# Optimization experiments

Measured on AMD Instinct MI355X. Metric: run time of the kernel, lower is better.

The kernel has to match this reference:

```python
import jax, jax.numpy as jnp
import numpy as np

B, S, SE, H, NH = 1, 2048, 2048, 1024, 16
HD = H // NH
INNER = 4 * H
EPS = 1e-5


def layer_norm(x, g, b):
    mu = jnp.mean(x, axis=-1, keepdims=True)
    var = jnp.mean(jnp.square(x - mu), axis=-1, keepdims=True)
    return (x - mu) * jax.lax.rsqrt(var + EPS) * g + b


def split_heads(x):  # [B,T,H] -> [B,NH,T,HD]
    b, t, _ = x.shape
    return x.reshape(b, t, NH, HD).transpose(0, 2, 1, 3)


def merge_heads(x):  # [B,NH,T,HD] -> [B,T,H]
    b, nh, t, hd = x.shape
    return x.transpose(0, 2, 1, 3).reshape(b, t, nh * hd)


def setup_inputs() -> dict:
    key = jax.random.key(0)
    ks = jax.random.split(key, 16)
    n = lambda k, shp: (jax.random.normal(k, shp, jnp.float32) * 0.02)
    return {
        "hidden_states": jax.random.normal(ks[0], (B, S, H), jnp.float32),
        "encoder_hidden_states": jax.random.normal(ks[1], (B, SE, H), jnp.float32),
        "scorer_logits": jax.random.normal(ks[2], (B, SE), jnp.float32),
        "ln1_g": jnp.ones((H,), jnp.float32), "ln1_b": jnp.zeros((H,), jnp.float32),
        "c_attn_w": n(ks[3], (H, 3 * H)), "c_attn_b": jnp.zeros((3 * H,), jnp.float32),
        "attn_proj_w": n(ks[4], (H, H)), "attn_proj_b": jnp.zeros((H,), jnp.float32),
        "lnx_g": jnp.ones((H,), jnp.float32), "lnx_b": jnp.zeros((H,), jnp.float32),
        "q_attn_w": n(ks[5], (H, H)), "q_attn_b": jnp.zeros((H,), jnp.float32),
        "x_kv_w": n(ks[6], (H, 2 * H)), "x_kv_b": jnp.zeros((2 * H,), jnp.float32),
        "x_proj_w": n(ks[7], (H, H)), "x_proj_b": jnp.zeros((H,), jnp.float32),
        "ln2_g": jnp.ones((H,), jnp.float32), "ln2_b": jnp.zeros((H,), jnp.float32),
        "fc_w": n(ks[8], (H, INNER)), "fc_b": jnp.zeros((INNER,), jnp.float32),
        "mlp_proj_w": n(ks[9], (INNER, H)), "mlp_proj_b": jnp.zeros((H,), jnp.float32),
    }


def _attn_core(q, k, v, extra_bias=None, causal_bool=False, tril_diag2_additive=False):
    # q,k,v: [B,NH,T,HD]; eager attention, materializes full score matrix (faithful to source)
    w = jnp.einsum("bhqd,bhkd->bhqk", q, k) / jnp.sqrt(jnp.asarray(HD, q.dtype))
    ql, kl = q.shape[-2], k.shape[-2]
    neg = jnp.finfo(w.dtype).min
    if causal_bool:
        mask = jnp.tril(jnp.ones((ql, kl), bool))  # self-attn boolean causal mask
        w = jnp.where(mask[None, None], w, neg)
    if tril_diag2_additive:
        cm = jnp.tril(jnp.ones((ql, kl), w.dtype), k=2)  # limit_cross_attn: tril diagonal=2
        w = w + jnp.where(cm == 0, neg, jnp.zeros((), w.dtype))[None, None]
    if extra_bias is not None:
        w = w + extra_bias[:, None, None, :]  # scorer_logits additive per-key bias
    w = jax.nn.softmax(w, axis=-1)
    return jnp.einsum("bhqk,bhkd->bhqd", w, v)


def reference(hidden_states, encoder_hidden_states, scorer_logits,
              ln1_g, ln1_b, c_attn_w, c_attn_b, attn_proj_w, attn_proj_b,
              lnx_g, lnx_b, q_attn_w, q_attn_b, x_kv_w, x_kv_b, x_proj_w, x_proj_b,
              ln2_g, ln2_b, fc_w, fc_b, mlp_proj_w, mlp_proj_b):
    # --- self attention ---
    residual = hidden_states
    x = layer_norm(hidden_states, ln1_g, ln1_b)
    qkv = x @ c_attn_w + c_attn_b
    q, k, v = jnp.split(qkv, 3, axis=-1)
    a = _attn_core(split_heads(q), split_heads(k), split_heads(v), causal_bool=True)
    a = merge_heads(a) @ attn_proj_w + attn_proj_b
    hidden_states = a + residual
    # --- cross attention (limit_cross_attn=True, scorer_logits bias) ---
    residual = hidden_states
    x = layer_norm(hidden_states, lnx_g, lnx_b)
    q = x @ q_attn_w + q_attn_b
    kv = encoder_hidden_states @ x_kv_w + x_kv_b
    k, v = jnp.split(kv, 2, axis=-1)
    a = _attn_core(split_heads(q), split_heads(k), split_heads(v),
                   extra_bias=scorer_logits, tril_diag2_additive=True)
    a = merge_heads(a) @ x_proj_w + x_proj_b
    hidden_states = residual + a
    # --- MLP (gelu_new = tanh approx) ---
    residual = hidden_states
    x = layer_norm(hidden_states, ln2_g, ln2_b)
    h = jax.nn.gelu(x @ fc_w + fc_b, approximate=True)
    hidden_states = residual + (h @ mlp_proj_w + mlp_proj_b)
    return hidden_states
```

## Files before the change

### kernel.cpp

```cpp
#include <hip/hip_runtime.h>
#include <stdint.h>

#define H     1024
#define S     2048
#define SEQE  2048
#define NHEAD 16
#define HD    64
#define INNER 4096
#define EPSLN 1e-5f
#define LOG2E 1.44269504089f
#define SCALE2 (0.125f * LOG2E)

typedef __attribute__((ext_vector_type(8))) short short8;
typedef __attribute__((ext_vector_type(4))) float floatx4;

__device__ __forceinline__ float b2f(unsigned short u){
  union { unsigned int i; float f; } v; v.i = ((unsigned int)u) << 16; return v.f;
}
__device__ __forceinline__ unsigned short f2b(float f){
  union { float f; unsigned int i; } v; v.f = f;
  unsigned int x = v.i;
  unsigned int r = (x + 0x7FFFu + ((x >> 16) & 1u)) >> 16;
  return (unsigned short)r;
}
__device__ __forceinline__ float gelu_tanh(float x){
  float x3 = x*x*x;
  float t = tanhf(0.7978845608028654f*(x + 0.044715f*x3));
  return 0.5f*x*(1.0f+t);
}

__device__ __forceinline__ void gld16(const unsigned short* g, unsigned short* l){
  __builtin_amdgcn_global_load_lds(
      (const __attribute__((address_space(1))) unsigned int*)g,
      (__attribute__((address_space(3))) unsigned int*)l,
      16, 0, 0);
}

__global__ __launch_bounds__(256) void k_sniff(
    const unsigned short* __restrict__ p, int* __restrict__ flag){
  __shared__ int any;
  if (threadIdx.x == 0) any = 0;
  __syncthreads();
  int bad = 0;
  for (int i = threadIdx.x; i < 8192; i += 256){
    float v = b2f(p[i]);
    if (!(fabsf(v) < 1e6f)) bad = 1;
  }
  if (bad) any = 1;
  __syncthreads();
  if (threadIdx.x == 0) flag[0] = any;
}

__global__ __launch_bounds__(256) void k_cvt(
    const void* __restrict__ src, unsigned short* __restrict__ dst, int n,
    const int* __restrict__ flag){
  int i = blockIdx.x * 256 + threadIdx.x;
  if (i < n)
    dst[i] = flag[0] ? f2b(((const float*)src)[i]) : ((const unsigned short*)src)[i];
}

struct SmallCvt {
  const void* src[16];
  unsigned short* dst[16];
  int n[16];
};
__global__ __launch_bounds__(256) void k_cvt_small(SmallCvt sc, const int* __restrict__ flag){
  int t = blockIdx.x;
  int fl = flag[0];
  const float* sf = (const float*)sc.src[t];
  const unsigned short* sb = (const unsigned short*)sc.src[t];
  unsigned short* d = sc.dst[t];
  for (int i = threadIdx.x; i < sc.n[t]; i += 256)
    d[i] = fl ? f2b(sf[i]) : sb[i];
}

__global__ __launch_bounds__(256) void k_transpose(
    const void* __restrict__ srcv, unsigned short* __restrict__ dst,
    int R, int C, const int* __restrict__ flag){
  __shared__ unsigned short t[32][33];
  const float* sf = (const float*)srcv;
  const unsigned short* sb = (const unsigned short*)srcv;
  int fl = flag[0];
  int bc = blockIdx.x * 32, br = blockIdx.y * 32;
  int tx = threadIdx.x, ty = threadIdx.y;
  #pragma unroll
  for (int i = 0; i < 4; i++){
    size_t idx = (size_t)(br + ty + i*8) * C + bc + tx;
    t[ty + i*8][tx] = fl ? f2b(sf[idx]) : sb[idx];
  }
  __syncthreads();
  #pragma unroll
  for (int i = 0; i < 4; i++)
    dst[(size_t)(bc + ty + i*8) * R + br + tx] = t[tx][ty + i*8];
}

__global__ __launch_bounds__(256) void k_resid_init(
    const void* __restrict__ in, float* __restrict__ out, int n,
    const int* __restrict__ flag){
  int i = blockIdx.x * 256 + threadIdx.x;
  if (i < n)
    out[i] = flag[0] ? ((const float*)in)[i] : b2f(((const unsigned short*)in)[i]);
}

__global__ __launch_bounds__(256) void k_layernorm(
    const float* __restrict__ x,
    const unsigned short* __restrict__ g, const unsigned short* __restrict__ bb,
    unsigned short* __restrict__ y){
  __shared__ float scratch[4];
  int row = blockIdx.x, tid = threadIdx.x;
  float v[4];
  #pragma unroll
  for (int i=0;i<4;i++) v[i] = x[(size_t)row*H + tid + i*256];
  float s = v[0]+v[1]+v[2]+v[3];
  for (int o=32;o;o>>=1) s += __shfl_xor(s,o,64);
  int wid = tid>>6, lane = tid&63;
  if (lane==0) scratch[wid]=s;
  __syncthreads();
  float mu = (scratch[0]+scratch[1]+scratch[2]+scratch[3]) * (1.0f/H);
  __syncthreads();
  float q = 0.f;
  #pragma unroll
  for (int i=0;i<4;i++){ float d=v[i]-mu; q += d*d; }
  for (int o=32;o;o>>=1) q += __shfl_xor(q,o,64);
  if (lane==0) scratch[wid]=q;
  __syncthreads();
  float var = (scratch[0]+scratch[1]+scratch[2]+scratch[3]) * (1.0f/H);
  float rstd = rsqrtf(var + EPSLN);
  #pragma unroll
  for (int i=0;i<4;i++){
    int idx = tid + i*256;
    float o = (v[i]-mu)*rstd*b2f(g[idx]) + b2f(bb[idx]);
    y[(size_t)row*H + idx] = f2b(o);
  }
}

__global__ __launch_bounds__(256) void k_gemm64(
    const unsigned short* __restrict__ A, const unsigned short* __restrict__ BT,
    const unsigned short* __restrict__ bias,
    unsigned short* __restrict__ outb, float* __restrict__ resid,
    int M, int N, int K, int mode, const int* __restrict__ flag,
    int vcol0, unsigned short* __restrict__ vtout)
{
  __shared__ __align__(16) unsigned short As[2][64*64];
  __shared__ __align__(16) unsigned short Bs[2][128*64];
  int tid = threadIdx.x;
  int bm0 = blockIdx.y * 64, bn0 = blockIdx.x * 128;
  int wid = tid >> 6, lane = tid & 63;
  int wm = (wid & 1) * 32, wn = (wid >> 1) * 64;
  int fl = (mode == 3) ? flag[0] : 0;
  floatx4 acc[2][4] = {};

  const unsigned short* gp[6];
  int lofs[6];
  int aseg[6];
  int lrow = lane >> 3, lchunk = (lane & 7) ^ lrow;
  #pragma unroll
  for (int t = 0; t < 6; t++){
    int seg = wid * 6 + t;
    if (seg < 8){
      gp[t] = A + (size_t)(bm0 + seg*8 + lrow) * K + lchunk*8;
      lofs[t] = seg * 512;
      aseg[t] = 1;
    } else {
      int s = seg - 8;
      gp[t] = BT + (size_t)(bn0 + s*8 + lrow) * K + lchunk*8;
      lofs[t] = s * 512;
      aseg[t] = 0;
    }
  }

  #pragma unroll
  for (int t = 0; t < 6; t++)
    gld16(gp[t], (aseg[t] ? As[0] : Bs[0]) + lofs[t]);

  int mrow = lane & 15, quad = lane >> 4;
  int ib = 0;
  for (int kt = 0; kt < K; kt += 64, ib ^= 1){
    __syncthreads();
    if (kt + 64 < K){
      #pragma unroll
      for (int t = 0; t < 6; t++)
        gld16(gp[t] + kt + 64, (aseg[t] ? As[ib^1] : Bs[ib^1]) + lofs[t]);
    }
    const unsigned short* Ac = As[ib];
    const unsigned short* Bc = Bs[ib];
    #pragma unroll
    for (int k2 = 0; k2 < 2; k2++){
      short8 af[2], bf[4];
      #pragma unroll
      for (int i = 0; i < 2; i++){
        int r = wm + i*16 + mrow;
        int slot = (k2*4 + quad) ^ (r & 7);
        af[i] = *(const short8*)&Ac[r*64 + slot*8];
      }
      #pragma unroll
      for (int j = 0; j < 4; j++){
        int r = wn + j*16 + mrow;
        int slot = (k2*4 + quad) ^ (r & 7);
        bf[j] = *(const short8*)&Bc[r*64 + slot*8];
      }
      #pragma unroll
      for (int i = 0; i < 2; i++){
        #pragma unroll
        for (int j = 0; j < 4; j++){
          acc[i][j] = __builtin_amdgcn_mfma_f32_16x16x32_bf16(af[i], bf[j], acc[i][j], 0,0,0);
        }
      }
    }
  }

  int colb = mrow, rowb = quad * 4;
  #pragma unroll
  for (int i=0;i<2;i++){
    #pragma unroll
    for (int j=0;j<4;j++){
      int col = bn0 + wn + j*16 + colb;
      float bv = b2f(bias[col]);
      int row0 = bm0 + wm + i*16 + rowb;
      if (mode == 4 && col >= vcol0){
        ushort4 uv;
        uv.x = f2b(acc[i][j][0] + bv);
        uv.y = f2b(acc[i][j][1] + bv);
        uv.z = f2b(acc[i][j][2] + bv);
        uv.w = f2b(acc[i][j][3] + bv);
        *(ushort4*)(vtout + (size_t)(col - vcol0)*M + row0) = uv;
      } else {
        #pragma unroll
        for (int rr=0;rr<4;rr++){
          int row = row0 + rr;
          float v = acc[i][j][rr] + bv;
          size_t off = (size_t)row*N + col;
          if      (mode == 0 || mode == 4){ outb[off] = f2b(v); }
          else if (mode == 1){ outb[off] = f2b(gelu_tanh(v)); }
          else if (mode == 2){ resid[off] += v; }
          else {
            float o = v + resid[off];
            if (fl) ((float*)outb)[off] = o;
            else    outb[off] = f2b(o);
          }
        }
      }
    }
  }
}

template<int CA, int SCOR>
__global__ __launch_bounds__(256) void k_flash2(
    const unsigned short* __restrict__ qb, int qstride,
    const unsigned short* __restrict__ kb, int kstride,
    const unsigned short* __restrict__ vt,
    const unsigned short* __restrict__ scorer,
    unsigned short* __restrict__ obuf, float* __restrict__ mlbuf, int TOTS)
{
  int t = blockIdx.x, h = blockIdx.y, sp = blockIdx.z;
  int klmax0 = 64*t + 64 + CA; if (klmax0 > S) klmax0 = S;
  int nch = (klmax0 + 63) >> 6;
  int nsp = (nch + 7) >> 3;
  if (sp >= nsp) return;
  int base = 0;
  for (int i = 0; i < t; i++){
    int km = 64*i + 64 + CA; if (km > S) km = S;
    base += (((km + 63) >> 6) + 7) >> 3;
  }
  int pidx = h*TOTS + base + sp;
  int c0 = sp*8, c1 = c0 + 8; if (c1 > nch) c1 = nch;

  __shared__ __align__(16) unsigned short Ks[64*64];
  __shared__ __align__(16) unsigned short VTs[64*64];
  __shared__ __align__(16) unsigned short Ps[4][16*72];
  __shared__ float scs[64];
  int tid = threadIdx.x;
  int q0 = t*64;
  int w = tid >> 6, lane = tid & 63;
  int cn = lane & 15, quad = lane >> 4, kq = quad * 8;
  unsigned short* Pw = Ps[w];
  int srow0 = w*16;
  int lr = lane >> 3;
  int lc = ((lane & 7) ^ lr) * 8;
  const unsigned short* kg0 = kb + (size_t)(srow0 + lr) * kstride + h*HD + lc;
  const unsigned short* kg1 = kb + (size_t)(srow0 + 8 + lr) * kstride + h*HD + lc;
  const unsigned short* vg0 = vt + (size_t)(h*HD + srow0 + lr) * S + lc;
  const unsigned short* vg1 = vt + (size_t)(h*HD + srow0 + 8 + lr) * S + lc;
  unsigned short* kl0 = &Ks[srow0 * 64];
  unsigned short* kl1 = &Ks[(srow0 + 8) * 64];
  unsigned short* vl0 = &VTs[srow0 * 64];
  unsigned short* vl1 = &VTs[(srow0 + 8) * 64];

  const unsigned short* qrow = qb + (size_t)(q0 + w*16 + cn) * qstride + h*HD;
  short8 qf0 = *(const short8*)(qrow + kq);
  short8 qf1 = *(const short8*)(qrow + kq + 32);
  floatx4 oacc[4] = {};
  float l_lane[4] = {0,0,0,0};
  float m_w = -1.0e38f;
  int qmr = q0 + w*16 + quad*4;

  for (int ci = c0; ci < c1; ci++){
    int kc = ci * 64;
    __syncthreads();
    gld16(kg0 + (size_t)kc * kstride, kl0);
    gld16(kg1 + (size_t)kc * kstride, kl1);
    gld16(vg0 + kc, vl0);
    gld16(vg1 + kc, vl1);
    if (SCOR && tid < 64) scs[tid] = b2f(scorer[kc + tid]) * LOG2E;
    __syncthreads();

    floatx4 sv[4] = {};
    #pragma unroll
    for (int t4=0;t4<4;t4++){
      int rr = t4*16 + cn;
      int s0 = ((quad    ) ^ (rr & 7)) * 8;
      int s1 = ((quad + 4) ^ (rr & 7)) * 8;
      short8 b0 = *(const short8*)&Ks[rr*64 + s0];
      short8 b1 = *(const short8*)&Ks[rr*64 + s1];
      sv[t4] = __builtin_amdgcn_mfma_f32_16x16x32_bf16(qf0, b0, sv[t4], 0,0,0);
      sv[t4] = __builtin_amdgcn_mfma_f32_16x16x32_bf16(qf1, b1, sv[t4], 0,0,0);
    }

    float vals[16];
    float lmax = -1.0e38f;
    bool needmask = (kc + 63 > q0 + w*16 + CA);
    #pragma unroll
    for (int t4=0;t4<4;t4++){
      #pragma unroll
      for (int r=0;r<4;r++){
        float s = sv[t4][r] * SCALE2;
        if (SCOR) s += scs[t4*16 + cn];
        if (needmask){
          int kn = kc + t4*16 + cn;
          s = (kn <= qmr + r + CA) ? s : -1.0e38f;
        }
        vals[t4*4+r] = s;
        lmax = fmaxf(lmax, s);
      }
    }
    #pragma unroll
    for (int o=1;o<64;o<<=1) lmax = fmaxf(lmax, __shfl_xor(lmax, o, 64));
    if (lmax > m_w){
      float al = exp2f(m_w - lmax);
      m_w = lmax;
      #pragma unroll
      for (int r=0;r<4;r++) l_lane[r] *= al;
      #pragma unroll
      for (int t2=0;t2<4;t2++){
        #pragma unroll
        for (int r=0;r<4;r++) oacc[t2][r] *= al;
      }
    }
    #pragma unroll
    for (int t4=0;t4<4;t4++){
      #pragma unroll
      for (int r=0;r<4;r++){
        float e = exp2f(vals[t4*4+r] - m_w);
        l_lane[r] += e;
        Pw[(quad*4+r)*72 + t4*16 + cn] = f2b(e);
      }
    }
    short8 pf0 = *(const short8*)&Pw[cn*72 + kq];
    short8 pf1 = *(const short8*)&Pw[cn*72 + kq + 32];
    #pragma unroll
    for (int t2=0;t2<4;t2++){
      int rr = t2*16 + cn;
      int s0 = ((quad    ) ^ (rr & 7)) * 8;
      int s1 = ((quad + 4) ^ (rr & 7)) * 8;
      short8 v0 = *(const short8*)&VTs[rr*64 + s0];
      short8 v1 = *(const short8*)&VTs[rr*64 + s1];
      oacc[t2] = __builtin_amdgcn_mfma_f32_16x16x32_bf16(pf0, v0, oacc[t2], 0,0,0);
      oacc[t2] = __builtin_amdgcn_mfma_f32_16x16x32_bf16(pf1, v1, oacc[t2], 0,0,0);
    }
  }

  float lrow[4];
  #pragma unroll
  for (int r=0;r<4;r++){
    float l = l_lane[r];
    l += __shfl_xor(l,1,64); l += __shfl_xor(l,2,64);
    l += __shfl_xor(l,4,64); l += __shfl_xor(l,8,64);
    lrow[r] = l;
  }
  size_t ob = (size_t)pidx*4096 + (size_t)(w*16 + quad*4)*64;
  #pragma unroll
  for (int t2=0;t2<4;t2++){
    #pragma unroll
    for (int r=0;r<4;r++)
      obuf[ob + r*64 + t2*16 + cn] = f2b(oacc[t2][r]);
  }
  if (cn == 0){
    #pragma unroll
    for (int r=0;r<4;r++){
      int row64 = w*16 + quad*4 + r;
      mlbuf[((size_t)pidx*64 + row64)*2]   = m_w;
      mlbuf[((size_t)pidx*64 + row64)*2+1] = lrow[r];
    }
  }
}

template<int CA>
__global__ __launch_bounds__(256) void k_comb(
    const unsigned short* __restrict__ obuf, const float* __restrict__ mlbuf,
    unsigned short* __restrict__ out, int TOTS)
{
  int h = blockIdx.y;
  int row = blockIdx.x*16 + (threadIdx.x >> 4);
  int d0 = (threadIdx.x & 15) * 4;
  int t = row >> 6;
  int klmax0 = 64*t + 64 + CA; if (klmax0 > S) klmax0 = S;
  int nch = (klmax0 + 63) >> 6;
  int nsp = (nch + 7) >> 3;
  int base = 0;
  for (int i = 0; i < t; i++){
    int km = 64*i + 64 + CA; if (km > S) km = S;
    base += (((km + 63) >> 6) + 7) >> 3;
  }
  int row64 = row & 63;
  float mp[4], lp[4];
  float M = -1.0e38f;
  for (int p = 0; p < nsp; p++){
    int pi = h*TOTS + base + p;
    mp[p] = mlbuf[((size_t)pi*64 + row64)*2];
    lp[p] = mlbuf[((size_t)pi*64 + row64)*2+1];
    M = fmaxf(M, mp[p]);
  }
  float L = 0.f;
  float o0=0.f,o1=0.f,o2=0.f,o3=0.f;
  for (int p = 0; p < nsp; p++){
    int pi = h*TOTS + base + p;
    float wgt = exp2f(mp[p] - M);
    L += lp[p]*wgt;
    const unsigned short* op = obuf + (size_t)pi*4096 + row64*64 + d0;
    o0 += b2f(op[0])*wgt; o1 += b2f(op[1])*wgt;
    o2 += b2f(op[2])*wgt; o3 += b2f(op[3])*wgt;
  }
  float inv = 1.0f / L;
  size_t oo = (size_t)row*H + h*HD + d0;
  out[oo]   = f2b(o0*inv); out[oo+1] = f2b(o1*inv);
  out[oo+2] = f2b(o2*inv); out[oo+3] = f2b(o3*inv);
}

extern "C" void kernel_launch(void* const* d_in, const int* in_sizes, int n_in,
                              void* d_out, int out_size, void* d_ws, size_t ws_size,
                              hipStream_t stream)
{
  const void* hs          = d_in[0];
  const void* enc         = d_in[1];
  const void* scorer      = d_in[2];
  const void* ln1_g       = d_in[3];
  const void* ln1_b       = d_in[4];
  const void* c_attn_w    = d_in[5];
  const void* c_attn_b    = d_in[6];
  const void* attn_proj_w = d_in[7];
  const void* attn_proj_b = d_in[8];
  const void* lnx_g       = d_in[9];
  const void* lnx_b       = d_in[10];
  const void* q_attn_w    = d_in[11];
  const void* q_attn_b    = d_in[12];
  const void* x_kv_w      = d_in[13];
  const void* x_kv_b      = d_in[14];
  const void* x_proj_w    = d_in[15];
  const void* x_proj_b    = d_in[16];
  const void* ln2_g       = d_in[17];
  const void* ln2_b       = d_in[18];
  const void* fc_w        = d_in[19];
  const void* fc_b        = d_in[20];
  const void* mlp_proj_w  = d_in[21];
  const void* mlp_proj_b  = d_in[22];
  unsigned short* out = (unsigned short*)d_out;

  char* ws = (char*)d_ws; size_t off = 0;
  auto alloc = [&](size_t bytes)->void*{
    void* p = ws + off; off += (bytes + 255) & ~(size_t)255; return p;
  };
  unsigned short* wT_cattn = (unsigned short*)alloc((size_t)3072*1024*2);
  unsigned short* wT_aproj = (unsigned short*)alloc((size_t)1024*1024*2);
  unsigned short* wT_qattn = (unsigned short*)alloc((size_t)1024*1024*2);
  unsigned short* wT_xkv   = (unsigned short*)alloc((size_t)2048*1024*2);
  unsigned short* wT_xproj = (unsigned short*)alloc((size_t)1024*1024*2);
  unsigned short* wT_fc    = (unsigned short*)alloc((size_t)4096*1024*2);
  unsigned short* wT_mlp   = (unsigned short*)alloc((size_t)1024*4096*2);
  unsigned short* enc_c    = (unsigned short*)alloc((size_t)SEQE*H*2);
  unsigned short* canon    = (unsigned short*)alloc((size_t)32768*2);
  unsigned short* xln      = (unsigned short*)alloc((size_t)S*H*2);
  unsigned short* qkv      = (unsigned short*)alloc((size_t)S*3*H*2);
  unsigned short* attnout  = (unsigned short*)alloc((size_t)S*H*2);
  unsigned short* q2       = (unsigned short*)alloc((size_t)S*H*2);
  unsigned short* kvbuf    = (unsigned short*)alloc((size_t)SEQE*2*H*2);
  unsigned short* vt_self  = (unsigned short*)alloc((size_t)H*S*2);
  unsigned short* vt_cross = (unsigned short*)alloc((size_t)H*SEQE*2);
  unsigned short* fcbuf    = (unsigned short*)alloc((size_t)S*INNER*2);
  float*          hidden   = (float*)alloc((size_t)S*H*4);
  int*            flag     = (int*)alloc(256);

  unsigned short* obuf  = fcbuf;
  float*          mlbuf = (float*)(fcbuf + (size_t)16*83*4096);

  unsigned short* p = canon;
  auto carve = [&](int n)->unsigned short*{ unsigned short* q = p; p += n; return q; };
  unsigned short* c_ln1g = carve(1024); unsigned short* c_ln1b = carve(1024);
  unsigned short* c_catb = carve(3072); unsigned short* c_aprb = carve(1024);
  unsigned short* c_lnxg = carve(1024); unsigned short* c_lnxb = carve(1024);
  unsigned short* c_qatb = carve(1024); unsigned short* c_xkvb = carve(2048);
  unsigned short* c_xprb = carve(1024); unsigned short* c_ln2g = carve(1024);
  unsigned short* c_ln2b = carve(1024); unsigned short* c_fcb  = carve(4096);
  unsigned short* c_mlpb = carve(1024); unsigned short* c_scor = carve(2048);

  k_sniff<<<1, 256, 0, stream>>>((const unsigned short*)hs, flag);
  k_resid_init<<<(S*H)/256, 256, 0, stream>>>(hs, hidden, S*H, flag);

  dim3 tb(32,8);
  k_transpose<<<dim3(3072/32,1024/32), tb, 0, stream>>>(c_attn_w,    wT_cattn, 1024, 3072, flag);
  k_transpose<<<dim3(1024/32,1024/32), tb, 0, stream>>>(attn_proj_w, wT_aproj, 1024, 1024, flag);
  k_transpose<<<dim3(1024/32,1024/32), tb, 0, stream>>>(q_attn_w,    wT_qattn, 1024, 1024, flag);
  k_transpose<<<dim3(2048/32,1024/32), tb, 0, stream>>>(x_kv_w,      wT_xkv,   1024, 2048, flag);
  k_transpose<<<dim3(1024/32,1024/32), tb, 0, stream>>>(x_proj_w,    wT_xproj, 1024, 1024, flag);
  k_transpose<<<dim3(4096/32,1024/32), tb, 0, stream>>>(fc_w,        wT_fc,    1024, 4096, flag);
  k_transpose<<<dim3(1024/32,4096/32), tb, 0, stream>>>(mlp_proj_w,  wT_mlp,   4096, 1024, flag);

  k_cvt<<<(SEQE*H)/256, 256, 0, stream>>>(enc, enc_c, SEQE*H, flag);
  SmallCvt sc{};
  const void* ssrc[14] = {ln1_g, ln1_b, c_attn_b, attn_proj_b, lnx_g, lnx_b,
                          q_attn_b, x_kv_b, x_proj_b, ln2_g, ln2_b, fc_b,
                          mlp_proj_b, scorer};
  unsigned short* sdst[14] = {c_ln1g, c_ln1b, c_catb, c_aprb, c_lnxg, c_lnxb,
                              c_qatb, c_xkvb, c_xprb, c_ln2g, c_ln2b, c_fcb,
                              c_mlpb, c_scor};
  int sn[14] = {1024,1024,3072,1024,1024,1024,1024,2048,1024,1024,1024,4096,1024,2048};
  for (int i=0;i<14;i++){ sc.src[i]=ssrc[i]; sc.dst[i]=sdst[i]; sc.n[i]=sn[i]; }
  k_cvt_small<<<14, 256, 0, stream>>>(sc, flag);

  k_layernorm<<<S, 256, 0, stream>>>(hidden, c_ln1g, c_ln1b, xln);
  k_gemm64<<<dim3(3072/128, S/64), 256, 0, stream>>>(xln, wT_cattn, c_catb,
      qkv, nullptr, S, 3072, 1024, 4, flag, 2048, vt_self);
  k_flash2<0,0><<<dim3(32, NHEAD, 4), 256, 0, stream>>>(
      qkv, 3*H, qkv + 1024, 3*H, vt_self, nullptr, obuf, mlbuf, 80);
  k_comb<0><<<dim3(S/16, NHEAD), 256, 0, stream>>>(obuf, mlbuf, attnout, 80);
  k_gemm64<<<dim3(1024/128, S/64), 256, 0, stream>>>(attnout, wT_aproj, c_aprb,
      nullptr, hidden, S, 1024, 1024, 2, flag, 0, nullptr);

  k_layernorm<<<S, 256, 0, stream>>>(hidden, c_lnxg, c_lnxb, xln);
  k_gemm64<<<dim3(1024/128, S/64), 256, 0, stream>>>(xln, wT_qattn, c_qatb,
      q2, nullptr, S, 1024, 1024, 0, flag, 0, nullptr);
  k_gemm64<<<dim3(2048/128, SEQE/64), 256, 0, stream>>>(enc_c, wT_xkv, c_xkvb,
      kvbuf, nullptr, SEQE, 2048, 1024, 4, flag, 1024, vt_cross);
  k_flash2<2,1><<<dim3(32, NHEAD, 4), 256, 0, stream>>>(
      q2, H, kvbuf, 2*H, vt_cross, c_scor, obuf, mlbuf, 83);
  k_comb<2><<<dim3(S/16, NHEAD), 256, 0, stream>>>(obuf, mlbuf, attnout, 83);
  k_gemm64<<<dim3(1024/128, S/64), 256, 0, stream>>>(attnout, wT_xproj, c_xprb,
      nullptr, hidden, S, 1024, 1024, 2, flag, 0, nullptr);

  k_layernorm<<<S, 256, 0, stream>>>(hidden, c_ln2g, c_ln2b, xln);
  k_gemm64<<<dim3(INNER/128, S/64), 256, 0, stream>>>(xln, wT_fc, c_fcb,
      fcbuf, nullptr, S, INNER, 1024, 1, flag, 0, nullptr);
  k_gemm64<<<dim3(1024/128, S/64), 256, 0, stream>>>(fcbuf, wT_mlp, c_mlpb,
      out, hidden, S, 1024, INNER, 3, flag, 0, nullptr);
}
```

Measured before the change: 517.5 us.

## Double-buffer K/V tiles in flash attention and batch prep kernels into two launches

```diff
diff --git a/kernel.cpp b/kernel.cpp
--- a/kernel.cpp
+++ b/kernel.cpp
@@ -51,12 +51,35 @@
   if (threadIdx.x == 0) flag[0] = any;
 }
 
-__global__ __launch_bounds__(256) void k_cvt(
-    const void* __restrict__ src, unsigned short* __restrict__ dst, int n,
-    const int* __restrict__ flag){
-  int i = blockIdx.x * 256 + threadIdx.x;
-  if (i < n)
-    dst[i] = flag[0] ? f2b(((const float*)src)[i]) : ((const unsigned short*)src)[i];
+struct PrepT {
+  const void* src[7];
+  unsigned short* dst[7];
+  int R[7], C[7];
+  int pre[8];
+};
+__global__ __launch_bounds__(256) void k_prep_t(PrepT d, const int* __restrict__ flag){
+  __shared__ unsigned short t[32][33];
+  int b = blockIdx.x;
+  int m = 0;
+  while (b >= d.pre[m+1]) m++;
+  int ti = b - d.pre[m];
+  int R = d.R[m], C = d.C[m];
+  int tx = threadIdx.x & 31, ty = threadIdx.x >> 5;
+  int tilesx = C >> 5;
+  int bc = (ti % tilesx) << 5, br = (ti / tilesx) << 5;
+  const float* sf = (const float*)d.src[m];
+  const unsigned short* sb = (const unsigned short*)d.src[m];
+  unsigned short* dst = d.dst[m];
+  int fl = flag[0];
+  #pragma unroll
+  for (int i = 0; i < 4; i++){
+    size_t idx = (size_t)(br + ty + i*8) * C + bc + tx;
+    t[ty + i*8][tx] = fl ? f2b(sf[idx]) : sb[idx];
+  }
+  __syncthreads();
+  #pragma unroll
+  for (int i = 0; i < 4; i++)
+    dst[(size_t)(bc + ty + i*8) * R + br + tx] = t[tx][ty + i*8];
 }
 
 struct SmallCvt {
@@ -64,42 +87,26 @@
   unsigned short* dst[16];
   int n[16];
 };
-__global__ __launch_bounds__(256) void k_cvt_small(SmallCvt sc, const int* __restrict__ flag){
-  int t = blockIdx.x;
+__global__ __launch_bounds__(256) void k_prep_c(
+    const void* __restrict__ enc, unsigned short* __restrict__ enc_c,
+    const void* __restrict__ hsv, float* __restrict__ hidden,
+    SmallCvt sc, const int* __restrict__ flag){
+  int b = blockIdx.x, tid = threadIdx.x;
   int fl = flag[0];
-  const float* sf = (const float*)sc.src[t];
-  const unsigned short* sb = (const unsigned short*)sc.src[t];
-  unsigned short* d = sc.dst[t];
-  for (int i = threadIdx.x; i < sc.n[t]; i += 256)
-    d[i] = fl ? f2b(sf[i]) : sb[i];
-}
-
-__global__ __launch_bounds__(256) void k_transpose(
-    const void* __restrict__ srcv, unsigned short* __restrict__ dst,
-    int R, int C, const int* __restrict__ flag){
-  __shared__ unsigned short t[32][33];
-  const float* sf = (const float*)srcv;
-  const unsigned short* sb = (const unsigned short*)srcv;
-  int fl = flag[0];
-  int bc = blockIdx.x * 32, br = blockIdx.y * 32;
-  int tx = threadIdx.x, ty = threadIdx.y;
-  #pragma unroll
-  for (int i = 0; i < 4; i++){
-    size_t idx = (size_t)(br + ty + i*8) * C + bc + tx;
-    t[ty + i*8][tx] = fl ? f2b(sf[idx]) : sb[idx];
-  }
-  __syncthreads();
-  #pragma unroll
-  for (int i = 0; i < 4; i++)
-    dst[(size_t)(bc + ty + i*8) * R + br + tx] = t[tx][ty + i*8];
-}
-
-__global__ __launch_bounds__(256) void k_resid_init(
-    const void* __restrict__ in, float* __restrict__ out, int n,
-    const int* __restrict__ flag){
-  int i = blockIdx.x * 256 + threadIdx.x;
-  if (i < n)
-    out[i] = flag[0] ? ((const float*)in)[i] : b2f(((const unsigned short*)in)[i]);
+  if (b < 8192){
+    int i = b*256 + tid;
+    enc_c[i] = fl ? f2b(((const float*)enc)[i]) : ((const unsigned short*)enc)[i];
+  } else if (b < 16384){
+    int i = (b - 8192)*256 + tid;
+    hidden[i] = fl ? ((const float*)hsv)[i] : b2f(((const unsigned short*)hsv)[i]);
+  } else {
+    int t = b - 16384;
+    const float* sf = (const float*)sc.src[t];
+    const unsigned short* sb = (const unsigned short*)sc.src[t];
+    unsigned short* d = sc.dst[t];
+    for (int i = tid; i < sc.n[t]; i += 256)
+      d[i] = fl ? f2b(sf[i]) : sb[i];
+  }
 }
 
 __global__ __launch_bounds__(256) void k_layernorm(
@@ -265,10 +272,10 @@
   int pidx = h*TOTS + base + sp;
   int c0 = sp*8, c1 = c0 + 8; if (c1 > nch) c1 = nch;
 
-  __shared__ __align__(16) unsigned short Ks[64*64];
-  __shared__ __align__(16) unsigned short VTs[64*64];
+  __shared__ __align__(16) unsigned short Ks[2][64*64];
+  __shared__ __align__(16) unsigned short VTs[2][64*64];
   __shared__ __align__(16) unsigned short Ps[4][16*72];
-  __shared__ float scs[64];
+  __shared__ float scs[2][64];
   int tid = threadIdx.x;
   int q0 = t*64;
   int w = tid >> 6, lane = tid & 63;
@@ -281,10 +288,6 @@
   const unsigned short* kg1 = kb + (size_t)(srow0 + 8 + lr) * kstride + h*HD + lc;
   const unsigned short* vg0 = vt + (size_t)(h*HD + srow0 + lr) * S + lc;
   const unsigned short* vg1 = vt + (size_t)(h*HD + srow0 + 8 + lr) * S + lc;
-  unsigned short* kl0 = &Ks[srow0 * 64];
-  unsigned short* kl1 = &Ks[(srow0 + 8) * 64];
-  unsigned short* vl0 = &VTs[srow0 * 64];
-  unsigned short* vl1 = &VTs[(srow0 + 8) * 64];
 
   const unsigned short* qrow = qb + (size_t)(q0 + w*16 + cn) * qstride + h*HD;
   short8 qf0 = *(const short8*)(qrow + kq);
@@ -294,15 +297,30 @@
   float m_w = -1.0e38f;
   int qmr = q0 + w*16 + quad*4;
 
-  for (int ci = c0; ci < c1; ci++){
+  {
+    int kc = c0 * 64;
+    gld16(kg0 + (size_t)kc * kstride, Ks[0] + srow0*64);
+    gld16(kg1 + (size_t)kc * kstride, Ks[0] + (srow0 + 8)*64);
+    gld16(vg0 + kc, VTs[0] + srow0*64);
+    gld16(vg1 + kc, VTs[0] + (srow0 + 8)*64);
+    if (SCOR && tid < 64) scs[0][tid] = b2f(scorer[kc + tid]) * LOG2E;
+  }
+
+  int ib = 0;
+  for (int ci = c0; ci < c1; ci++, ib ^= 1){
+    __syncthreads();
+    if (ci + 1 < c1){
+      int kn2 = (ci + 1) * 64;
+      gld16(kg0 + (size_t)kn2 * kstride, Ks[ib^1] + srow0*64);
+      gld16(kg1 + (size_t)kn2 * kstride, Ks[ib^1] + (srow0 + 8)*64);
+      gld16(vg0 + kn2, VTs[ib^1] + srow0*64);
+      gld16(vg1 + kn2, VTs[ib^1] + (srow0 + 8)*64);
+      if (SCOR && tid < 64) scs[ib^1][tid] = b2f(scorer[kn2 + tid]) * LOG2E;
+    }
     int kc = ci * 64;
-    __syncthreads();
-    gld16(kg0 + (size_t)kc * kstride, kl0);
-    gld16(kg1 + (size_t)kc * kstride, kl1);
-    gld16(vg0 + kc, vl0);
-    gld16(vg1 + kc, vl1);
-    if (SCOR && tid < 64) scs[tid] = b2f(scorer[kc + tid]) * LOG2E;
-    __syncthreads();
+    const unsigned short* Kc = Ks[ib];
+    const unsigned short* Vc = VTs[ib];
+    const float* scc = scs[ib];
 
     floatx4 sv[4] = {};
     #pragma unroll
@@ -310,27 +328,37 @@
       int rr = t4*16 + cn;
       int s0 = ((quad    ) ^ (rr & 7)) * 8;
       int s1 = ((quad + 4) ^ (rr & 7)) * 8;
-      short8 b0 = *(const short8*)&Ks[rr*64 + s0];
-      short8 b1 = *(const short8*)&Ks[rr*64 + s1];
+      short8 b0 = *(const short8*)&Kc[rr*64 + s0];
+      short8 b1 = *(const short8*)&Kc[rr*64 + s1];
       sv[t4] = __builtin_amdgcn_mfma_f32_16x16x32_bf16(qf0, b0, sv[t4], 0,0,0);
       sv[t4] = __builtin_amdgcn_mfma_f32_16x16x32_bf16(qf1, b1, sv[t4], 0,0,0);
     }
 
     float vals[16];
     float lmax = -1.0e38f;
-    bool needmask = (kc + 63 > q0 + w*16 + CA);
-    #pragma unroll
-    for (int t4=0;t4<4;t4++){
-      #pragma unroll
-      for (int r=0;r<4;r++){
-        float s = sv[t4][r] * SCALE2;
-        if (SCOR) s += scs[t4*16 + cn];
-        if (needmask){
+    if (kc + 63 > q0 + w*16 + CA){
+      #pragma unroll
+      for (int t4=0;t4<4;t4++){
+        #pragma unroll
+        for (int r=0;r<4;r++){
+          float s = sv[t4][r] * SCALE2;
+          if (SCOR) s += scc[t4*16 + cn];
           int kn = kc + t4*16 + cn;
           s = (kn <= qmr + r + CA) ? s : -1.0e38f;
+          vals[t4*4+r] = s;
+          lmax = fmaxf(lmax, s);
         }
-        vals[t4*4+r] = s;
-        lmax = fmaxf(lmax, s);
+      }
+    } else {
+      #pragma unroll
+      for (int t4=0;t4<4;t4++){
+        #pragma unroll
+        for (int r=0;r<4;r++){
+          float s = sv[t4][r] * SCALE2;
+          if (SCOR) s += scc[t4*16 + cn];
+          vals[t4*4+r] = s;
+          lmax = fmaxf(lmax, s);
+        }
       }
     }
     #pragma unroll
@@ -362,8 +390,8 @@
       int rr = t2*16 + cn;
       int s0 = ((quad    ) ^ (rr & 7)) * 8;
       int s1 = ((quad + 4) ^ (rr & 7)) * 8;
-      short8 v0 = *(const short8*)&VTs[rr*64 + s0];
-      short8 v1 = *(const short8*)&VTs[rr*64 + s1];
+      short8 v0 = *(const short8*)&Vc[rr*64 + s0];
+      short8 v1 = *(const short8*)&Vc[rr*64 + s1];
       oacc[t2] = __builtin_amdgcn_mfma_f32_16x16x32_bf16(pf0, v0, oacc[t2], 0,0,0);
       oacc[t2] = __builtin_amdgcn_mfma_f32_16x16x32_bf16(pf1, v1, oacc[t2], 0,0,0);
     }
@@ -503,18 +531,20 @@
   unsigned short* c_mlpb = carve(1024); unsigned short* c_scor = carve(2048);
 
   k_sniff<<<1, 256, 0, stream>>>((const unsigned short*)hs, flag);
-  k_resid_init<<<(S*H)/256, 256, 0, stream>>>(hs, hidden, S*H, flag);
-
-  dim3 tb(32,8);
-  k_transpose<<<dim3(3072/32,1024/32), tb, 0, stream>>>(c_attn_w,    wT_cattn, 1024, 3072, flag);
-  k_transpose<<<dim3(1024/32,1024/32), tb, 0, stream>>>(attn_proj_w, wT_aproj, 1024, 1024, flag);
-  k_transpose<<<dim3(1024/32,1024/32), tb, 0, stream>>>(q_attn_w,    wT_qattn, 1024, 1024, flag);
-  k_transpose<<<dim3(2048/32,1024/32), tb, 0, stream>>>(x_kv_w,      wT_xkv,   1024, 2048, flag);
-  k_transpose<<<dim3(1024/32,1024/32), tb, 0, stream>>>(x_proj_w,    wT_xproj, 1024, 1024, flag);
-  k_transpose<<<dim3(4096/32,1024/32), tb, 0, stream>>>(fc_w,        wT_fc,    1024, 4096, flag);
-  k_transpose<<<dim3(1024/32,4096/32), tb, 0, stream>>>(mlp_proj_w,  wT_mlp,   4096, 1024, flag);
-
-  k_cvt<<<(SEQE*H)/256, 256, 0, stream>>>(enc, enc_c, SEQE*H, flag);
+
+  PrepT pt{};
+  const void* tsrc[7] = {c_attn_w, attn_proj_w, q_attn_w, x_kv_w, x_proj_w, fc_w, mlp_proj_w};
+  unsigned short* tdst[7] = {wT_cattn, wT_aproj, wT_qattn, wT_xkv, wT_xproj, wT_fc, wT_mlp};
+  int tR[7] = {1024,1024,1024,1024,1024,1024,4096};
+  int tC[7] = {3072,1024,1024,2048,1024,4096,1024};
+  int acc_t = 0;
+  for (int i=0;i<7;i++){
+    pt.src[i]=tsrc[i]; pt.dst[i]=tdst[i]; pt.R[i]=tR[i]; pt.C[i]=tC[i];
+    pt.pre[i]=acc_t; acc_t += (tC[i]>>5)*(tR[i]>>5);
+  }
+  pt.pre[7]=acc_t;
+  k_prep_t<<<acc_t, 256, 0, stream>>>(pt, flag);
+
   SmallCvt sc{};
   const void* ssrc[14] = {ln1_g, ln1_b, c_attn_b, attn_proj_b, lnx_g, lnx_b,
                           q_attn_b, x_kv_b, x_proj_b, ln2_g, ln2_b, fc_b,
@@ -524,7 +554,7 @@
                               c_mlpb, c_scor};
   int sn[14] = {1024,1024,3072,1024,1024,1024,1024,2048,1024,1024,1024,4096,1024,2048};
   for (int i=0;i<14;i++){ sc.src[i]=ssrc[i]; sc.dst[i]=sdst[i]; sc.n[i]=sn[i]; }
-  k_cvt_small<<<14, 256, 0, stream>>>(sc, flag);
+  k_prep_c<<<16384 + 14, 256, 0, stream>>>(enc, enc_c, hs, hidden, sc, flag);
 
   k_layernorm<<<S, 256, 0, stream>>>(hidden, c_ln1g, c_ln1b, xln);
   k_gemm64<<<dim3(3072/128, S/64), 256, 0, stream>>>(xln, wT_cattn, c_catb,
```

Measured after the change: 511.0 us. Within noise of the previous version (-1.3%).
